# Kernel tuning notes

Hardware: AMD Instinct MI355X
Metric: run time of the kernel (lower is better)

The kernel has to match this reference:

```python
import jax, jax.numpy as jnp
import numpy as np

D_MODEL, D_STATE, D_CONV, D_INNER = 1024, 16, 4, 2048
BATCH, SEQ = 4, 2048


def silu(v):
    return v * jax.nn.sigmoid(v)


def setup_inputs() -> dict:
    key = jax.random.key(0)
    ks = jax.random.split(key, 7)
    x = jax.random.normal(ks[0], (BATCH, SEQ, D_MODEL), dtype=jnp.float32)
    s = 0.02
    W_in = jax.random.normal(ks[1], (D_MODEL, 2 * D_INNER), dtype=jnp.float32) * s
    conv_w = jax.random.normal(ks[2], (D_INNER, 1, D_CONV), dtype=jnp.float32) * s  # depthwise (O, I/g=1, K)
    conv_b = jax.random.normal(ks[3], (D_INNER,), dtype=jnp.float32) * s
    W_xproj = jax.random.normal(ks[4], (D_INNER, 2 * D_STATE + 1), dtype=jnp.float32) * s
    A_log = jnp.log(jnp.tile(jnp.arange(1, D_STATE + 1, dtype=jnp.float32), (D_INNER, 1)))
    D = jnp.ones((D_INNER,), dtype=jnp.float32)
    W_out = jax.random.normal(ks[5], (D_INNER, D_MODEL), dtype=jnp.float32) * s
    return {"x": x, "W_in": W_in, "conv_w": conv_w, "conv_b": conv_b,
            "W_xproj": W_xproj, "A_log": A_log, "D": D, "W_out": W_out}


def reference(x, W_in, conv_w, conv_b, W_xproj, A_log, D, W_out):
    B, L, _ = x.shape
    xz = x @ W_in                                   # (B, L, 2*d_inner)
    x_proj, z = jnp.split(xz, 2, axis=-1)
    # Depthwise causal conv: padding=d_conv-1 then truncate to L == left-pad only.
    xc = jax.lax.conv_general_dilated(
        x_proj.transpose(0, 2, 1), conv_w,
        window_strides=(1,), padding=[(D_CONV - 1, 0)],
        feature_group_count=D_INNER,
        dimension_numbers=("NCH", "OIH", "NCH"))
    x_conv = silu((xc + conv_b[None, :, None]).transpose(0, 2, 1))  # (B, L, d_inner)
    ssm = x_conv @ W_xproj                           # (B, L, 1+2*d_state)
    delta = jax.nn.softplus(ssm[..., 0])             # (B, L)
    Bm = ssm[..., 1:1 + D_STATE]                     # (B, L, d_state)
    Cm = ssm[..., 1 + D_STATE:]                      # (B, L, d_state)
    # Original: deltaA = exp(delta*A) and softmax weights are computed but unused.
    deltaB = delta[..., None] * Bm                   # (B, L, d_state)
    # h_approx = mean_L(x outer deltaB): avoid (B,L,d_inner,d_state) intermediate.
    h_mean = jnp.einsum("bld,bln->bdn", x_conv, deltaB) / L  # (B, d_inner, d_state)
    y = jnp.einsum("bdn,bln->bld", h_mean, Cm)       # (B, L, d_inner)
    y = y + D[None, None, :] * x_conv
    y = y * silu(z)
    return y @ W_out                                 # (B, L, d_model)
```

## Files before the change

kernel.cpp:

```cpp
#include <hip/hip_runtime.h>
#include <hip/hip_bf16.h>
#include <stdint.h>

typedef __bf16 bf16x8 __attribute__((ext_vector_type(8)));
typedef float f32x4 __attribute__((ext_vector_type(4)));
typedef unsigned short u16;
typedef u16 ushort4v __attribute__((ext_vector_type(4)));
typedef u16 ushort8v __attribute__((ext_vector_type(8)));

__device__ __forceinline__ u16 f2bf(float f) {
    union { float f; uint32_t u; } v; v.f = f;
    uint32_t u = v.u + 0x7FFFu + ((v.u >> 16) & 1u);
    return (u16)(u >> 16);
}
__device__ __forceinline__ float bf2f(u16 b) {
    union { uint32_t u; float f; } v; v.u = ((uint32_t)b) << 16;
    return v.f;
}
__device__ __forceinline__ float silu_f(float v) {
    return v / (1.0f + __expf(-v));
}
__device__ __forceinline__ void gload_lds16(const u16* g, u16* l) {
    __builtin_amdgcn_global_load_lds(
        (const __attribute__((address_space(1))) void*)g,
        (__attribute__((address_space(3))) void*)l, 16, 0, 0);
}
__device__ __forceinline__ bf16x8 lds_read16(uint32_t addr) {
    bf16x8 r;
    asm volatile("ds_read_b128 %0, %1" : "=v"(r) : "v"(addr));
    return r;
}

__device__ __forceinline__ void trans_tile(
        const float* __restrict__ src, u16* __restrict__ dst, int R, int C,
        int bc, int br, float (*tt)[33], int tid) {
    const int tx = tid & 31, ty = tid >> 5;
#pragma unroll
    for (int i = 0; i < 4; i++)
        tt[ty + i * 8][tx] = src[(int64_t)(br * 32 + ty + i * 8) * C + bc * 32 + tx];
    __syncthreads();
#pragma unroll
    for (int i = 0; i < 4; i++)
        dst[(int64_t)(bc * 32 + ty + i * 8) * R + br * 32 + tx] = f2bf(tt[tx][ty + i * 8]);
}

__global__ __launch_bounds__(256) void prep_k(
        const float* __restrict__ x, u16* __restrict__ x_bf,
        const float* __restrict__ Wi, u16* __restrict__ Wti,
        const float* __restrict__ Wo, u16* __restrict__ Wto,
        const float* __restrict__ wx, u16* __restrict__ wxt) {
    __shared__ float tt[32][33];
    const int blk = blockIdx.x, tid = threadIdx.x;
    if (blk < 8192) {
        int i = blk * 256 + tid;
        float4 v = *(const float4*)&x[(int64_t)i * 4];
        ushort4v o = { f2bf(v.x), f2bf(v.y), f2bf(v.z), f2bf(v.w) };
        *(ushort4v*)&x_bf[(int64_t)i * 4] = o;
    } else if (blk < 12288) {
        int t = blk - 8192;
        trans_tile(Wi, Wti, 1024, 4096, t & 127, t >> 7, tt, tid);
    } else if (blk < 14336) {
        int t = blk - 12288;
        trans_tile(Wo, Wto, 2048, 1024, t & 31, t >> 5, tt, tid);
    } else {
        int idx = (blk - 14336) * 256 + tid;
        int j = idx >> 11, d = idx & 2047;
        wxt[idx] = (j < 33) ? f2bf(wx[d * 33 + j]) : (u16)0;
    }
}

template<int M_REP, int WARPS_M, int B_HALVES, bool OUT_BF16>
__global__ __launch_bounds__(512) void gemm_dp(
        const u16* __restrict__ A, const u16* __restrict__ Bt,
        void* __restrict__ Cout, int nbn_sh, int NT, int lda, int ldb, int ldc) {
    constexpr int WARPS_N = 8 / WARPS_M;
    constexpr int QPT = M_REP / 2;
    constexpr int WV_M = M_REP * 16;
    constexpr int BN = WARPS_N * 64;
    constexpr int B_T = BN * 64;

    __shared__ __align__(16) u16 As[2 * 16384];
    __shared__ __align__(16) u16 Bs[2 * B_T];
    const uint32_t asb = (uint32_t)(uintptr_t)&As[0];
    const uint32_t bsb = (uint32_t)(uintptr_t)&Bs[0];

    const int tid = threadIdx.x;
    const int wave = tid >> 6;
    const int lane = tid & 63;
    const int wm = wave / WARPS_N, wn = wave % WARPS_N;
    const int fr = lane & 15, fq = lane >> 4;

    const int nwg = gridDim.x;
    const int cpx = nwg >> 3;
    const int swz = (blockIdx.x & 7) * cpx + (blockIdx.x >> 3);
    const int bm = swz >> nbn_sh;
    const int bn = swz & ((1 << nbn_sh) - 1);

    const int srow = tid >> 3;
    const int scol8 = ((tid & 7) ^ (srow & 7)) * 8;
    const u16* gA = A + (int64_t)(bm * 256 + srow) * lda + scol8;
    const u16* gB = Bt + (int64_t)(bn * BN + srow) * ldb + scol8;
    const int64_t lda64 = lda, ldb64 = ldb;

    const int ksw0 = ((fq) ^ (fr & 7)) * 8;
    const int ksw1 = ((4 + fq) ^ (fr & 7)) * 8;
    const int arow0 = (wm * WV_M + fr) * 64;
    const int brow0 = (wn * 64 + fr) * 64;

    auto STAGE_A_HALF = [&](int kt, int buf, int h) {
#pragma unroll
        for (int j = 0; j < 2; ++j)
            gload_lds16(gA + (int64_t)(h * 128 + j * 64) * lda64 + kt * 64,
                        &As[buf * 16384 + h * 8192 + j * 4096 + tid * 8]);
    };
    auto STAGE_B_HALF = [&](int kt, int buf, int h) {
#pragma unroll
        for (int j = 0; j < 2; ++j)
            gload_lds16(gB + (int64_t)(h * 128 + j * 64) * ldb64 + kt * 64,
                        &Bs[buf * B_T + h * 8192 + j * 4096 + tid * 8]);
    };

    f32x4 acc[M_REP][4] = {};

    STAGE_A_HALF(0, 0, 0); STAGE_A_HALF(0, 0, 1);
#pragma unroll
    for (int h = 0; h < B_HALVES; ++h) STAGE_B_HALF(0, 0, h);
#pragma unroll
    for (int h = 0; h < B_HALVES; ++h) STAGE_B_HALF(1, 1, h);
    if constexpr (B_HALVES == 2) { asm volatile("s_waitcnt vmcnt(4)" ::: "memory"); }
    else                         { asm volatile("s_waitcnt vmcnt(2)" ::: "memory"); }
    __builtin_amdgcn_s_barrier();

    const int NI = NT >> 1;
    for (int s = 0; s < NI; ++s) {
        const bool more = (s + 1 < NI);
#pragma unroll
        for (int t = 0; t < 2; ++t) {
            const uint32_t Ab = asb + t * 32768u;
            const uint32_t Bb = bsb + t * (uint32_t)(B_T * 2);
            bf16x8 breg[4][2];
#pragma unroll
            for (int q = 0; q < QPT; ++q) {
                if (q == 0) {
#pragma unroll
                    for (int n = 0; n < 4; ++n) {
                        breg[n][0] = lds_read16(Bb + (uint32_t)(brow0 + n * 1024 + ksw0) * 2);
                        breg[n][1] = lds_read16(Bb + (uint32_t)(brow0 + n * 1024 + ksw1) * 2);
                    }
                }
                bf16x8 areg[2][2];
#pragma unroll
                for (int j = 0; j < 2; ++j) {
                    areg[j][0] = lds_read16(Ab + (uint32_t)(arow0 + (2 * q + j) * 1024 + ksw0) * 2);
                    areg[j][1] = lds_read16(Ab + (uint32_t)(arow0 + (2 * q + j) * 1024 + ksw1) * 2);
                }
                if constexpr (QPT == 4) {
                    if (t == 0 && q == 0)         STAGE_A_HALF(2 * s + 1, 1, 0);
                    if (t == 0 && q == 1)         STAGE_A_HALF(2 * s + 1, 1, 1);
                    if (t == 0 && q == 2 && more) STAGE_B_HALF(2 * s + 2, 0, 0);
                    if (t == 0 && q == 3 && more) STAGE_B_HALF(2 * s + 2, 0, 1);
                    if (t == 1 && q == 0 && more) STAGE_A_HALF(2 * s + 2, 0, 0);
                    if (t == 1 && q == 1 && more) STAGE_A_HALF(2 * s + 2, 0, 1);
                    if (t == 1 && q == 2 && more) STAGE_B_HALF(2 * s + 3, 1, 0);
                    if (t == 1 && q == 3 && more) STAGE_B_HALF(2 * s + 3, 1, 1);
                } else {
                    if (t == 0 && q == 0)         STAGE_A_HALF(2 * s + 1, 1, 0);
                    if (t == 0 && q == 1) {       STAGE_A_HALF(2 * s + 1, 1, 1);
                        if (more)                 STAGE_B_HALF(2 * s + 2, 0, 0); }
                    if (t == 1 && q == 0 && more) STAGE_A_HALF(2 * s + 2, 0, 0);
                    if (t == 1 && q == 1 && more) { STAGE_A_HALF(2 * s + 2, 0, 1);
                                                    STAGE_B_HALF(2 * s + 3, 1, 0); }
                }
                __builtin_amdgcn_s_barrier();
                asm volatile("s_waitcnt lgkmcnt(0)" ::: "memory");
                __builtin_amdgcn_sched_barrier(0);
                __builtin_amdgcn_s_setprio(1);
#pragma unroll
                for (int j = 0; j < 2; ++j)
#pragma unroll
                    for (int n = 0; n < 4; ++n) {
                        acc[2 * q + j][n] = __builtin_amdgcn_mfma_f32_16x16x32_bf16(
                            areg[j][0], breg[n][0], acc[2 * q + j][n], 0, 0, 0);
                        acc[2 * q + j][n] = __builtin_amdgcn_mfma_f32_16x16x32_bf16(
                            areg[j][1], breg[n][1], acc[2 * q + j][n], 0, 0, 0);
                    }
                __builtin_amdgcn_s_setprio(0);
                __builtin_amdgcn_sched_barrier(0);
                if (q == QPT - 1) {
                    if (more) {
                        if constexpr (B_HALVES == 2) { asm volatile("s_waitcnt vmcnt(4)" ::: "memory"); }
                        else                         { asm volatile("s_waitcnt vmcnt(2)" ::: "memory"); }
                    } else {
                        asm volatile("s_waitcnt vmcnt(0)" ::: "memory");
                    }
                }
                __builtin_amdgcn_s_barrier();
            }
        }
    }

#pragma unroll
    for (int m = 0; m < M_REP; ++m) {
#pragma unroll
        for (int n = 0; n < 4; ++n) {
            const int col = bn * BN + wn * 64 + n * 16 + fr;
#pragma unroll
            for (int r = 0; r < 4; ++r) {
                const int row = bm * 256 + wm * WV_M + m * 16 + fq * 4 + r;
                if constexpr (OUT_BF16)
                    ((u16*)Cout)[(int64_t)row * ldc + col] = f2bf(acc[m][n][r]);
                else
                    ((float*)Cout)[(int64_t)row * ldc + col] = acc[m][n][r];
            }
        }
    }
}

__global__ __launch_bounds__(256) void conv_silu_k(
        const u16* __restrict__ xz, const float* __restrict__ cw,
        const float* __restrict__ cb, u16* __restrict__ xc) {
    const int blk = blockIdx.x;
    const int b = blk >> 9;
    const int l0 = (blk & 511) << 2;
    const int d0 = threadIdx.x * 8;
    float w[8][4], bias[8];
#pragma unroll
    for (int j = 0; j < 8; j++) {
        float4 wv = *(const float4*)&cw[(d0 + j) * 4];
        w[j][0] = wv.x; w[j][1] = wv.y; w[j][2] = wv.z; w[j][3] = wv.w;
        bias[j] = cb[d0 + j];
    }
    float xp[7][8];
#pragma unroll
    for (int r = 0; r < 7; r++) {
        int l = l0 - 3 + r;
        if (l < 0) {
#pragma unroll
            for (int j = 0; j < 8; j++) xp[r][j] = 0.f;
        } else {
            ushort8v v = *(const ushort8v*)&xz[((int64_t)(b * 2048 + l)) * 4096 + d0];
#pragma unroll
            for (int j = 0; j < 8; j++) xp[r][j] = bf2f(v[j]);
        }
    }
#pragma unroll
    for (int li = 0; li < 4; li++) {
        ushort8v o;
#pragma unroll
        for (int j = 0; j < 8; j++) {
            float s = bias[j];
#pragma unroll
            for (int k = 0; k < 4; k++) s += w[j][k] * xp[li + k][j];
            o[j] = f2bf(silu_f(s));
        }
        *(ushort8v*)&xc[((int64_t)(b * 2048 + l0 + li)) * 2048 + d0] = o;
    }
}

__global__ __launch_bounds__(256) void ssm_proj_k(
        const u16* __restrict__ xc, const u16* __restrict__ wxt,
        float* __restrict__ spart) {
    const int gw = (blockIdx.x << 2) + (threadIdx.x >> 6);
    const int lane = threadIdx.x & 63;
    const int rb = gw >> 2, kc = gw & 3;
    const int fr = lane & 15, fq = lane >> 4;
    const u16* ap = xc + (int64_t)(rb * 16 + fr) * 2048 + kc * 512 + fq * 8;
    const u16* bp = wxt + (int64_t)fr * 2048 + kc * 512 + fq * 8;
    f32x4 acc0 = {}, acc1 = {}, acc2 = {};
#pragma unroll 4
    for (int k = 0; k < 512; k += 32) {
        bf16x8 av = *(const bf16x8*)(ap + k);
        bf16x8 b0 = *(const bf16x8*)(bp + k);
        bf16x8 b1 = *(const bf16x8*)(bp + 16 * 2048 + k);
        bf16x8 b2 = *(const bf16x8*)(bp + 32 * 2048 + k);
        acc0 = __builtin_amdgcn_mfma_f32_16x16x32_bf16(av, b0, acc0, 0, 0, 0);
        acc1 = __builtin_amdgcn_mfma_f32_16x16x32_bf16(av, b1, acc1, 0, 0, 0);
        acc2 = __builtin_amdgcn_mfma_f32_16x16x32_bf16(av, b2, acc2, 0, 0, 0);
    }
    float* sp = spart + ((int64_t)kc * 8192 + rb * 16) * 48;
#pragma unroll
    for (int r = 0; r < 4; r++) {
        int ro = (fq * 4 + r) * 48;
        sp[ro + fr] = acc0[r];
        sp[ro + 16 + fr] = acc1[r];
        sp[ro + 32 + fr] = acc2[r];
    }
}

__global__ __launch_bounds__(256) void ssm_fin_k(
        const float* __restrict__ spart, float* __restrict__ dB,
        float* __restrict__ Cm) {
    const int row = blockIdx.x * 256 + threadIdx.x;
    const float* sp = spart + (int64_t)row * 48;
    float s[33];
#pragma unroll
    for (int j = 0; j < 33; j++)
        s[j] = sp[j] + sp[8192 * 48 + j] + sp[2 * 8192 * 48 + j] + sp[3 * 8192 * 48 + j];
    float d0v = s[0];
    float delta = (d0v > 20.f) ? d0v : log1pf(__expf(d0v));
#pragma unroll
    for (int n = 0; n < 16; n++) {
        dB[(int64_t)row * 16 + n] = delta * s[1 + n] * (1.0f / 2048.0f);
        Cm[(int64_t)row * 16 + n] = s[17 + n];
    }
}

__global__ __launch_bounds__(256) void h_part_k(
        const u16* __restrict__ xc, const float* __restrict__ dB,
        float* __restrict__ hp) {
    const int blk = blockIdx.x;
    const int dt = blk & 7, b = (blk >> 3) & 3, lc = blk >> 5;
    const int d = dt * 256 + threadIdx.x;
    const u16* xp = xc + ((int64_t)(b * 2048 + lc * 256)) * 2048 + d;
    const float* dbp = dB + (int64_t)(b * 2048 + lc * 256) * 16;
    float acc[16] = {};
    for (int l = 0; l < 256; l++) {
        float xv = bf2f(xp[(int64_t)l * 2048]);
#pragma unroll
        for (int n = 0; n < 16; n++) acc[n] += xv * dbp[l * 16 + n];
    }
    float* o = hp + ((int64_t)((lc * 4 + b) * 2048 + d)) * 16;
#pragma unroll
    for (int n = 0; n < 16; n++) o[n] = acc[n];
}

__global__ void h_red_k(const float* __restrict__ hp, float* __restrict__ h) {
    const int i = blockIdx.x * 256 + threadIdx.x;
    float s = 0.f;
#pragma unroll
    for (int c = 0; c < 8; c++) s += hp[(int64_t)c * 131072 + i];
    h[i] = s;
}

__global__ __launch_bounds__(256) void y_gate_k(
        u16* __restrict__ xz, const u16* __restrict__ xc,
        const float* __restrict__ h, const float* __restrict__ Cm,
        const float* __restrict__ Dp) {
    const int blk = blockIdx.x;
    const int lc = blk & 63, dt = (blk >> 6) & 1, b = blk >> 7;
    const int d0 = dt * 1024 + threadIdx.x * 4;
    const float* hpp = h + ((int64_t)(b * 2048 + d0)) * 16;
    float hreg[4][16];
#pragma unroll
    for (int i = 0; i < 4; i++)
#pragma unroll
        for (int n = 0; n < 16; n++) hreg[i][n] = hpp[i * 16 + n];
    float Dv[4];
#pragma unroll
    for (int i = 0; i < 4; i++) Dv[i] = Dp[d0 + i];
    __shared__ float Cs[32][16];
    if (threadIdx.x < 128)
        ((float4*)&Cs[0][0])[threadIdx.x] =
            ((const float4*)(Cm + (int64_t)(b * 2048 + lc * 32) * 16))[threadIdx.x];
    __syncthreads();
    for (int li = 0; li < 32; li++) {
        const int64_t rowz = (int64_t)(b * 2048 + lc * 32 + li);
        ushort4v xcv = *(const ushort4v*)&xc[rowz * 2048 + d0];
        ushort4v zv = *(const ushort4v*)&xz[rowz * 4096 + 2048 + d0];
        ushort4v o;
#pragma unroll
        for (int i = 0; i < 4; i++) {
            float s = Dv[i] * bf2f(xcv[i]);
#pragma unroll
            for (int n = 0; n < 16; n++) s += hreg[i][n] * Cs[li][n];
            o[i] = f2bf(s * silu_f(bf2f(zv[i])));
        }
        *(ushort4v*)&xz[rowz * 4096 + d0] = o;
    }
}

extern "C" void kernel_launch(void* const* d_in, const int* in_sizes, int n_in,
                              void* d_out, int out_size, void* d_ws, size_t ws_size,
                              hipStream_t stream) {
    (void)in_sizes; (void)n_in; (void)out_size; (void)ws_size;
    const float* x      = (const float*)d_in[0];
    const float* W_in   = (const float*)d_in[1];
    const float* conv_w = (const float*)d_in[2];
    const float* conv_b = (const float*)d_in[3];
    const float* W_xp   = (const float*)d_in[4];
    const float* Dp     = (const float*)d_in[6];
    const float* W_out  = (const float*)d_in[7];
    float* out = (float*)d_out;
    char* ws = (char*)d_ws;

    u16*   x_bf   = (u16*)(ws);
    float* spart  = (float*)(ws);
    float* dB     = (float*)(ws + 6291456);
    float* Cm     = (float*)(ws + 6815744);
    float* hp     = (float*)(ws + 7340032);
    float* h      = (float*)(ws + 11534336);
    u16*   Wt_in  = (u16*)(ws + 16777216);
    u16*   Wt_out = (u16*)(ws + 25165824);
    u16*   Wxt    = (u16*)(ws + 29360128);
    u16*   xz     = (u16*)(ws + 29556736);
    u16*   xcv    = (u16*)(ws + 96665600);

    prep_k<<<14720, 256, 0, stream>>>(x, x_bf, W_in, Wt_in, W_out, Wt_out, W_xp, Wxt);
    gemm_dp<8, 2, 2, true><<<512, 512, 0, stream>>>(x_bf, Wt_in, xz, 4, 16, 1024, 1024, 4096);
    conv_silu_k<<<2048, 256, 0, stream>>>(xz, conv_w, conv_b, xcv);
    ssm_proj_k<<<512, 256, 0, stream>>>(xcv, Wxt, spart);
    ssm_fin_k<<<32, 256, 0, stream>>>(spart, dB, Cm);
    h_part_k<<<256, 256, 0, stream>>>(xcv, dB, hp);
    h_red_k<<<512, 256, 0, stream>>>(hp, h);
    y_gate_k<<<512, 256, 0, stream>>>(xz, xcv, h, Cm, Dp);
    gemm_dp<4, 4, 1, false><<<256, 512, 0, stream>>>(xz, Wt_out, out, 3, 32, 4096, 2048, 1024);
}
```

Measured before the change: 244.1 us.

## Rewrite GEMM main loop as triple-buffered BK=32 pipeline; split h reduction finer

Replaces the GEMM's double-buffered BK=64 loop, which used hand-interleaved half-tile staging and inline-asm LDS reads, with a simpler triple-buffered BK=32 loop. Each iteration prefetches two tiles ahead, reads fragments with plain vector loads and issues one MFMA per fragment pair. The aim is better overlap of global loads with compute, at the cost of twice as many barriers and waits per K. Separately, the h partial reduction is split over 32 length chunks instead of 8 to raise parallelism, and ssm_fin uses smaller blocks to spread across more CUs.

Result: slower. 261.6 us (+7.2%).

```diff
diff --git a/kernel.cpp b/kernel.cpp
--- a/kernel.cpp
+++ b/kernel.cpp
@@ -24,11 +24,6 @@
     __builtin_amdgcn_global_load_lds(
         (const __attribute__((address_space(1))) void*)g,
         (__attribute__((address_space(3))) void*)l, 16, 0, 0);
-}
-__device__ __forceinline__ bf16x8 lds_read16(uint32_t addr) {
-    bf16x8 r;
-    asm volatile("ds_read_b128 %0, %1" : "=v"(r) : "v"(addr));
-    return r;
 }
 
 __device__ __forceinline__ void trans_tile(
@@ -69,20 +64,18 @@
     }
 }
 
-template<int M_REP, int WARPS_M, int B_HALVES, bool OUT_BF16>
+template<int M_REP, int WARPS_M, int B_SLOTS, bool OUT_BF16>
 __global__ __launch_bounds__(512) void gemm_dp(
         const u16* __restrict__ A, const u16* __restrict__ Bt,
         void* __restrict__ Cout, int nbn_sh, int NT, int lda, int ldb, int ldc) {
     constexpr int WARPS_N = 8 / WARPS_M;
-    constexpr int QPT = M_REP / 2;
     constexpr int WV_M = M_REP * 16;
     constexpr int BN = WARPS_N * 64;
-    constexpr int B_T = BN * 64;
-
-    __shared__ __align__(16) u16 As[2 * 16384];
-    __shared__ __align__(16) u16 Bs[2 * B_T];
-    const uint32_t asb = (uint32_t)(uintptr_t)&As[0];
-    const uint32_t bsb = (uint32_t)(uintptr_t)&Bs[0];
+    constexpr int B_T = BN * 32;
+    constexpr int VK = 2 + B_SLOTS;
+
+    __shared__ __align__(16) u16 As[3 * 8192];
+    __shared__ __align__(16) u16 Bs[3 * B_T];
 
     const int tid = threadIdx.x;
     const int wave = tid >> 6;
@@ -96,107 +89,65 @@
     const int bm = swz >> nbn_sh;
     const int bn = swz & ((1 << nbn_sh) - 1);
 
-    const int srow = tid >> 3;
-    const int scol8 = ((tid & 7) ^ (srow & 7)) * 8;
-    const u16* gA = A + (int64_t)(bm * 256 + srow) * lda + scol8;
-    const u16* gB = Bt + (int64_t)(bn * BN + srow) * ldb + scol8;
+    const int srow = tid >> 2;
+    const int sc = (((tid & 3) ^ ((tid >> 3) & 3)) << 3);
+    const u16* gA = A + (int64_t)(bm * 256 + srow) * lda + sc;
+    const u16* gB = Bt + (int64_t)(bn * BN + srow) * ldb + sc;
     const int64_t lda64 = lda, ldb64 = ldb;
 
-    const int ksw0 = ((fq) ^ (fr & 7)) * 8;
-    const int ksw1 = ((4 + fq) ^ (fr & 7)) * 8;
-    const int arow0 = (wm * WV_M + fr) * 64;
-    const int brow0 = (wn * 64 + fr) * 64;
-
-    auto STAGE_A_HALF = [&](int kt, int buf, int h) {
+    const int arow0 = wm * WV_M + fr;
+    const int brow0 = wn * 64 + fr;
+    const int aswz = ((fq ^ ((arow0 >> 1) & 3)) << 3);
+    const int bswz = ((fq ^ ((brow0 >> 1) & 3)) << 3);
+
+    auto STAGE = [&](int kt) {
+        const int bi = kt % 3;
 #pragma unroll
         for (int j = 0; j < 2; ++j)
-            gload_lds16(gA + (int64_t)(h * 128 + j * 64) * lda64 + kt * 64,
-                        &As[buf * 16384 + h * 8192 + j * 4096 + tid * 8]);
+            gload_lds16(gA + (int64_t)(j * 128) * lda64 + kt * 32,
+                        &As[bi * 8192 + j * 4096 + tid * 8]);
+#pragma unroll
+        for (int j = 0; j < B_SLOTS; ++j)
+            gload_lds16(gB + (int64_t)(j * 128) * ldb64 + kt * 32,
+                        &Bs[bi * B_T + j * 4096 + tid * 8]);
     };
-    auto STAGE_B_HALF = [&](int kt, int buf, int h) {
-#pragma unroll
-        for (int j = 0; j < 2; ++j)
-            gload_lds16(gB + (int64_t)(h * 128 + j * 64) * ldb64 + kt * 64,
-                        &Bs[buf * B_T + h * 8192 + j * 4096 + tid * 8]);
-    };
 
     f32x4 acc[M_REP][4] = {};
 
-    STAGE_A_HALF(0, 0, 0); STAGE_A_HALF(0, 0, 1);
-#pragma unroll
-    for (int h = 0; h < B_HALVES; ++h) STAGE_B_HALF(0, 0, h);
-#pragma unroll
-    for (int h = 0; h < B_HALVES; ++h) STAGE_B_HALF(1, 1, h);
-    if constexpr (B_HALVES == 2) { asm volatile("s_waitcnt vmcnt(4)" ::: "memory"); }
-    else                         { asm volatile("s_waitcnt vmcnt(2)" ::: "memory"); }
+    STAGE(0); STAGE(1);
+    if constexpr (B_SLOTS == 2) { asm volatile("s_waitcnt vmcnt(4)" ::: "memory"); }
+    else                        { asm volatile("s_waitcnt vmcnt(3)" ::: "memory"); }
     __builtin_amdgcn_s_barrier();
-
-    const int NI = NT >> 1;
-    for (int s = 0; s < NI; ++s) {
-        const bool more = (s + 1 < NI);
-#pragma unroll
-        for (int t = 0; t < 2; ++t) {
-            const uint32_t Ab = asb + t * 32768u;
-            const uint32_t Bb = bsb + t * (uint32_t)(B_T * 2);
-            bf16x8 breg[4][2];
-#pragma unroll
-            for (int q = 0; q < QPT; ++q) {
-                if (q == 0) {
-#pragma unroll
-                    for (int n = 0; n < 4; ++n) {
-                        breg[n][0] = lds_read16(Bb + (uint32_t)(brow0 + n * 1024 + ksw0) * 2);
-                        breg[n][1] = lds_read16(Bb + (uint32_t)(brow0 + n * 1024 + ksw1) * 2);
-                    }
-                }
-                bf16x8 areg[2][2];
-#pragma unroll
-                for (int j = 0; j < 2; ++j) {
-                    areg[j][0] = lds_read16(Ab + (uint32_t)(arow0 + (2 * q + j) * 1024 + ksw0) * 2);
-                    areg[j][1] = lds_read16(Ab + (uint32_t)(arow0 + (2 * q + j) * 1024 + ksw1) * 2);
-                }
-                if constexpr (QPT == 4) {
-                    if (t == 0 && q == 0)         STAGE_A_HALF(2 * s + 1, 1, 0);
-                    if (t == 0 && q == 1)         STAGE_A_HALF(2 * s + 1, 1, 1);
-                    if (t == 0 && q == 2 && more) STAGE_B_HALF(2 * s + 2, 0, 0);
-                    if (t == 0 && q == 3 && more) STAGE_B_HALF(2 * s + 2, 0, 1);
-                    if (t == 1 && q == 0 && more) STAGE_A_HALF(2 * s + 2, 0, 0);
-                    if (t == 1 && q == 1 && more) STAGE_A_HALF(2 * s + 2, 0, 1);
-                    if (t == 1 && q == 2 && more) STAGE_B_HALF(2 * s + 3, 1, 0);
-                    if (t == 1 && q == 3 && more) STAGE_B_HALF(2 * s + 3, 1, 1);
-                } else {
-                    if (t == 0 && q == 0)         STAGE_A_HALF(2 * s + 1, 1, 0);
-                    if (t == 0 && q == 1) {       STAGE_A_HALF(2 * s + 1, 1, 1);
-                        if (more)                 STAGE_B_HALF(2 * s + 2, 0, 0); }
-                    if (t == 1 && q == 0 && more) STAGE_A_HALF(2 * s + 2, 0, 0);
-                    if (t == 1 && q == 1 && more) { STAGE_A_HALF(2 * s + 2, 0, 1);
-                                                    STAGE_B_HALF(2 * s + 3, 1, 0); }
-                }
-                __builtin_amdgcn_s_barrier();
-                asm volatile("s_waitcnt lgkmcnt(0)" ::: "memory");
-                __builtin_amdgcn_sched_barrier(0);
-                __builtin_amdgcn_s_setprio(1);
-#pragma unroll
-                for (int j = 0; j < 2; ++j)
-#pragma unroll
-                    for (int n = 0; n < 4; ++n) {
-                        acc[2 * q + j][n] = __builtin_amdgcn_mfma_f32_16x16x32_bf16(
-                            areg[j][0], breg[n][0], acc[2 * q + j][n], 0, 0, 0);
-                        acc[2 * q + j][n] = __builtin_amdgcn_mfma_f32_16x16x32_bf16(
-                            areg[j][1], breg[n][1], acc[2 * q + j][n], 0, 0, 0);
-                    }
-                __builtin_amdgcn_s_setprio(0);
-                __builtin_amdgcn_sched_barrier(0);
-                if (q == QPT - 1) {
-                    if (more) {
-                        if constexpr (B_HALVES == 2) { asm volatile("s_waitcnt vmcnt(4)" ::: "memory"); }
-                        else                         { asm volatile("s_waitcnt vmcnt(2)" ::: "memory"); }
-                    } else {
-                        asm volatile("s_waitcnt vmcnt(0)" ::: "memory");
-                    }
-                }
-                __builtin_amdgcn_s_barrier();
-            }
-        }
+    asm volatile("" ::: "memory");
+
+    for (int kt = 0; kt < NT; ++kt) {
+        if (kt + 2 < NT) STAGE(kt + 2);
+        const int ab = (kt % 3) * 8192;
+        const int bb = (kt % 3) * B_T;
+        bf16x8 ar[M_REP], br[4];
+#pragma unroll
+        for (int m = 0; m < M_REP; ++m)
+            ar[m] = *(const bf16x8*)&As[ab + (arow0 + m * 16) * 32 + aswz];
+#pragma unroll
+        for (int n = 0; n < 4; ++n)
+            br[n] = *(const bf16x8*)&Bs[bb + (brow0 + n * 16) * 32 + bswz];
+        __builtin_amdgcn_s_setprio(1);
+#pragma unroll
+        for (int m = 0; m < M_REP; ++m)
+#pragma unroll
+            for (int n = 0; n < 4; ++n)
+                acc[m][n] = __builtin_amdgcn_mfma_f32_16x16x32_bf16(ar[m], br[n], acc[m][n], 0, 0, 0);
+        __builtin_amdgcn_s_setprio(0);
+        asm volatile("s_waitcnt lgkmcnt(0)" ::: "memory");
+        __builtin_amdgcn_sched_barrier(0);
+        if (kt + 2 < NT) {
+            if constexpr (B_SLOTS == 2) { asm volatile("s_waitcnt vmcnt(4)" ::: "memory"); }
+            else                        { asm volatile("s_waitcnt vmcnt(3)" ::: "memory"); }
+        } else {
+            asm volatile("s_waitcnt vmcnt(0)" ::: "memory");
+        }
+        __builtin_amdgcn_s_barrier();
+        asm volatile("" ::: "memory");
     }
 
 #pragma unroll
@@ -287,10 +238,10 @@
     }
 }
 
-__global__ __launch_bounds__(256) void ssm_fin_k(
+__global__ __launch_bounds__(64) void ssm_fin_k(
         const float* __restrict__ spart, float* __restrict__ dB,
         float* __restrict__ Cm) {
-    const int row = blockIdx.x * 256 + threadIdx.x;
+    const int row = blockIdx.x * 64 + threadIdx.x;
     const float* sp = spart + (int64_t)row * 48;
     float s[33];
 #pragma unroll
@@ -311,10 +262,10 @@
     const int blk = blockIdx.x;
     const int dt = blk & 7, b = (blk >> 3) & 3, lc = blk >> 5;
     const int d = dt * 256 + threadIdx.x;
-    const u16* xp = xc + ((int64_t)(b * 2048 + lc * 256)) * 2048 + d;
-    const float* dbp = dB + (int64_t)(b * 2048 + lc * 256) * 16;
+    const u16* xp = xc + ((int64_t)(b * 2048 + lc * 64)) * 2048 + d;
+    const float* dbp = dB + (int64_t)(b * 2048 + lc * 64) * 16;
     float acc[16] = {};
-    for (int l = 0; l < 256; l++) {
+    for (int l = 0; l < 64; l++) {
         float xv = bf2f(xp[(int64_t)l * 2048]);
 #pragma unroll
         for (int n = 0; n < 16; n++) acc[n] += xv * dbp[l * 16 + n];
@@ -328,7 +279,7 @@
     const int i = blockIdx.x * 256 + threadIdx.x;
     float s = 0.f;
 #pragma unroll
-    for (int c = 0; c < 8; c++) s += hp[(int64_t)c * 131072 + i];
+    for (int c = 0; c < 32; c++) s += hp[(int64_t)c * 131072 + i];
     h[i] = s;
 }
 
@@ -387,8 +338,8 @@
     float* spart  = (float*)(ws);
     float* dB     = (float*)(ws + 6291456);
     float* Cm     = (float*)(ws + 6815744);
-    float* hp     = (float*)(ws + 7340032);
-    float* h      = (float*)(ws + 11534336);
+    float* h      = (float*)(ws + 7340032);
+    float* hp     = (float*)(ws + 7864320);
     u16*   Wt_in  = (u16*)(ws + 16777216);
     u16*   Wt_out = (u16*)(ws + 25165824);
     u16*   Wxt    = (u16*)(ws + 29360128);
@@ -396,12 +347,12 @@
     u16*   xcv    = (u16*)(ws + 96665600);
 
     prep_k<<<14720, 256, 0, stream>>>(x, x_bf, W_in, Wt_in, W_out, Wt_out, W_xp, Wxt);
-    gemm_dp<8, 2, 2, true><<<512, 512, 0, stream>>>(x_bf, Wt_in, xz, 4, 16, 1024, 1024, 4096);
+    gemm_dp<8, 2, 2, true><<<512, 512, 0, stream>>>(x_bf, Wt_in, xz, 4, 32, 1024, 1024, 4096);
     conv_silu_k<<<2048, 256, 0, stream>>>(xz, conv_w, conv_b, xcv);
     ssm_proj_k<<<512, 256, 0, stream>>>(xcv, Wxt, spart);
-    ssm_fin_k<<<32, 256, 0, stream>>>(spart, dB, Cm);
-    h_part_k<<<256, 256, 0, stream>>>(xcv, dB, hp);
+    ssm_fin_k<<<128, 64, 0, stream>>>(spart, dB, Cm);
+    h_part_k<<<1024, 256, 0, stream>>>(xcv, dB, hp);
     h_red_k<<<512, 256, 0, stream>>>(hp, h);
     y_gate_k<<<512, 256, 0, stream>>>(xz, xcv, h, Cm, Dp);
-    gemm_dp<4, 4, 1, false><<<256, 512, 0, stream>>>(xz, Wt_out, out, 3, 32, 4096, 2048, 1024);
-}
+    gemm_dp<4, 4, 1, false><<<256, 512, 0, stream>>>(xz, Wt_out, out, 3, 64, 4096, 2048, 1024);
+}
```
